# Kernel tuning notes

Measured on AMD Instinct MI355X. Metric: run time of the kernel, lower is better.

Reference implementation:

```python
import jax, jax.numpy as jnp
import numpy as np

B = 16384
TEXT_D = 768
TECH_D = 256
IN_D = TEXT_D + TECH_D  # 1024
OUT_D = 1024
E = 8


def setup_inputs() -> dict:
    key = jax.random.key(0)
    ks = jax.random.split(key, 8)
    s_in = 1.0 / np.sqrt(IN_D)
    s_out = 1.0 / np.sqrt(OUT_D)
    return {
        "text_features": jax.random.normal(ks[0], (B, TEXT_D), jnp.float32),
        "technical_features": jax.random.normal(ks[1], (B, TECH_D), jnp.float32),
        # stacked expert params: layer1 [E, IN_D, OUT_D], layer2 [E, OUT_D, OUT_D]
        "W1": jax.random.uniform(ks[2], (E, IN_D, OUT_D), jnp.float32, -s_in, s_in),
        "b1": jax.random.uniform(ks[3], (E, OUT_D), jnp.float32, -s_in, s_in),
        "W2": jax.random.uniform(ks[4], (E, OUT_D, OUT_D), jnp.float32, -s_out, s_out),
        "b2": jax.random.uniform(ks[5], (E, OUT_D), jnp.float32, -s_out, s_out),
        # gating network
        "Wg": jax.random.uniform(ks[6], (IN_D, E), jnp.float32, -s_in, s_in),
        "bg": jax.random.uniform(ks[7], (E,), jnp.float32, -s_in, s_in),
    }


def reference(text_features, technical_features, W1, b1, W2, b2, Wg, bg):
    x = jnp.concatenate([text_features, technical_features], axis=-1)  # [B, IN_D]
    gates = jax.nn.softmax(x @ Wg + bg, axis=-1)                       # [B, E]
    h = jax.nn.relu(jnp.einsum('bi,eio->beo', x, W1) + b1[None])       # [B, E, OUT_D]
    y = jnp.einsum('beo,eop->bep', h, W2) + b2[None]                   # [B, E, OUT_D]
    return jnp.einsum('be,bep->bp', gates, y)                          # [B, OUT_D]
```

## Files before the change

kernel.cpp:

```cpp
#include <hip/hip_runtime.h>
#include <hip/hip_bf16.h>

#define NB 16384
#define TEXT_D 768
#define TECH_D 256
#define IND 1024
#define OUTD 1024
#define NE 8
#define KH2 4096

typedef unsigned short u16;
typedef __bf16 bf16x8 __attribute__((ext_vector_type(8)));
typedef float f32x4 __attribute__((ext_vector_type(4)));

__device__ __forceinline__ u16 f2bf(float f) {
  union { float f; unsigned int u; } x; x.f = f;
  unsigned int u = x.u;
  return (u16)((u + 0x7FFFu + ((u >> 16) & 1u)) >> 16);
}

__device__ __forceinline__ void gload_lds16(const void* g, void* l) {
  __builtin_amdgcn_global_load_lds(
      (const __attribute__((address_space(1))) unsigned int*)g,
      (__attribute__((address_space(3))) unsigned int*)l, 16, 0, 0);
}

__global__ __launch_bounds__(256) void convert_gates(
    const float* __restrict__ text, const float* __restrict__ tech,
    const float* __restrict__ Wg, const float* __restrict__ bg,
    u16* __restrict__ xb, float* __restrict__ gates) {
  int t = threadIdx.x;
  int wave = t >> 6, lane = t & 63;
  int row = blockIdx.x * 4 + wave;

  float acc[NE];
#pragma unroll
  for (int e = 0; e < NE; ++e) acc[e] = 0.f;

#pragma unroll
  for (int j = 0; j < 4; ++j) {
    int col = j * 256 + lane * 4;
    float4 v = (j < 3) ? *(const float4*)&text[(size_t)row * TEXT_D + col]
                       : *(const float4*)&tech[(size_t)row * TECH_D + lane * 4];
    ushort4 o = make_ushort4(f2bf(v.x), f2bf(v.y), f2bf(v.z), f2bf(v.w));
    *(ushort4*)&xb[(size_t)row * IND + col] = o;
    const float* wp = &Wg[(size_t)col * NE];
    float xv[4] = {v.x, v.y, v.z, v.w};
#pragma unroll
    for (int i = 0; i < 4; ++i) {
      float4 w0 = *(const float4*)&wp[i * NE];
      float4 w1 = *(const float4*)&wp[i * NE + 4];
      acc[0] = fmaf(xv[i], w0.x, acc[0]);
      acc[1] = fmaf(xv[i], w0.y, acc[1]);
      acc[2] = fmaf(xv[i], w0.z, acc[2]);
      acc[3] = fmaf(xv[i], w0.w, acc[3]);
      acc[4] = fmaf(xv[i], w1.x, acc[4]);
      acc[5] = fmaf(xv[i], w1.y, acc[5]);
      acc[6] = fmaf(xv[i], w1.z, acc[6]);
      acc[7] = fmaf(xv[i], w1.w, acc[7]);
    }
  }
#pragma unroll
  for (int off = 32; off; off >>= 1)
#pragma unroll
    for (int e = 0; e < NE; ++e) acc[e] += __shfl_xor(acc[e], off);

#pragma unroll
  for (int e = 0; e < NE; ++e) acc[e] += bg[e];
  float mx = acc[0];
#pragma unroll
  for (int e = 1; e < NE; ++e) mx = fmaxf(mx, acc[e]);
  float s = 0.f;
#pragma unroll
  for (int e = 0; e < NE; ++e) { acc[e] = expf(acc[e] - mx); s += acc[e]; }
  float inv = 1.f / s;
  if (lane < NE) gates[(size_t)row * NE + lane] = acc[lane] * inv;
}

__global__ __launch_bounds__(256) void transpose_w12(
    const float* __restrict__ W1, const float* __restrict__ W2,
    u16* __restrict__ W1t, u16* __restrict__ W2t) {
  __shared__ u16 tile[64][65];
  int bid = blockIdx.x;
  int half = bid >> 11;
  int b2 = bid & 2047;
  int e = b2 >> 8;
  int tb = b2 & 255;
  int r0 = (tb >> 4) * 64;
  int c0 = (tb & 15) * 64;
  const float* We; u16* Wte; int ostride;
  if (half == 0) {
    We = W1 + (size_t)e * IND * OUTD;
    Wte = W1t + ((size_t)e << 20);
    ostride = 1024;
  } else {
    We = W2 + (size_t)e * IND * OUTD;
    Wte = W2t + ((size_t)(e >> 2) << 22) + (size_t)(e & 3) * 1024;
    ostride = KH2;
  }
  int t = threadIdx.x;
  int tr = t >> 4;
  int s  = t & 15;
  int tc = s * 4;
#pragma unroll
  for (int j = 0; j < 4; ++j) {
    int row = j * 16 + tr;
    float4 v = *(const float4*)&We[(size_t)(r0 + row) * OUTD + c0 + tc];
    tile[row][tc + 0] = f2bf(v.x);
    tile[row][tc + 1] = f2bf(v.y);
    tile[row][tc + 2] = f2bf(v.z);
    tile[row][tc + 3] = f2bf(v.w);
  }
  __syncthreads();
#pragma unroll
  for (int j = 0; j < 4; ++j) {
    int row = j * 16 + tr;
    ushort4 o;
    if (half == 0) {
      o = make_ushort4(tile[tc + 0][row], tile[tc + 1][row],
                       tile[tc + 2][row], tile[tc + 3][row]);
    } else {
      o = make_ushort4(tile[s][row], tile[s + 16][row],
                       tile[s + 32][row], tile[s + 48][row]);
    }
    *(ushort4*)&Wte[(size_t)(c0 + row) * ostride + r0 + tc] = o;
  }
}

#define BAR() asm volatile("s_barrier" ::: "memory")
#define VM0() asm volatile("s_waitcnt vmcnt(0)" ::: "memory")
#define VM2() asm volatile("s_waitcnt vmcnt(2)" ::: "memory")
#define VM6() asm volatile("s_waitcnt vmcnt(6)" ::: "memory")

template <int SLOT, int K>
__device__ __forceinline__ void stage_slot(
    const u16* __restrict__ g, char* buf, int k0,
    int ch0, int rsub, int koff, int lbyte) {
#pragma unroll
  for (int j = 0; j < 2; ++j) {
    int ch = ch0 + j;
    int r;
    if constexpr (SLOT == 0)      r = (ch >> 3) * 128 + (ch & 7) * 8 + rsub;
    else if constexpr (SLOT == 3) r = 64 + (ch >> 3) * 128 + (ch & 7) * 8 + rsub;
    else if constexpr (SLOT == 1) r = (ch >> 2) * 64 + (ch & 3) * 8 + rsub;
    else                          r = (ch >> 2) * 64 + 32 + (ch & 3) * 8 + rsub;
    gload_lds16(g + (size_t)r * K + k0 + koff, buf + r * 128 + lbyte);
  }
}

template <int QH>
__device__ __forceinline__ void load_a(const char* rb, int wr, int lr, int hi,
                                       int swr, bf16x8 (&a)[4][2]) {
#pragma unroll
  for (int i = 0; i < 4; ++i)
#pragma unroll
    for (int ks = 0; ks < 2; ++ks)
      a[i][ks] = *(const bf16x8*)(rb + (wr * 128 + QH * 64 + i * 16 + lr) * 128
                                  + ((ks * 64 + hi * 16) ^ swr));
}

template <int NH>
__device__ __forceinline__ void load_b(const char* rb, int wc, int lr, int hi,
                                       int swr, bf16x8 (&b)[2][2]) {
#pragma unroll
  for (int q = 0; q < 2; ++q)
#pragma unroll
    for (int ks = 0; ks < 2; ++ks)
      b[q][ks] = *(const bf16x8*)(rb +
                                  (wc * 64 + (NH * 2 + q) * 16 + lr) * 128
                                  + ((ks * 64 + hi * 16) ^ swr));
}

template <int MH, int NH>
__device__ __forceinline__ void mfma_quad(const bf16x8 (&a)[4][2],
                                          const bf16x8 (&b)[2][2],
                                          f32x4 (&acc)[8][4]) {
#pragma unroll
  for (int i = 0; i < 4; ++i)
#pragma unroll
    for (int q = 0; q < 2; ++q) {
      acc[MH*4+i][NH*2+q] = __builtin_amdgcn_mfma_f32_16x16x32_bf16(
          a[i][0], b[q][0], acc[MH*4+i][NH*2+q], 0, 0, 0);
      acc[MH*4+i][NH*2+q] = __builtin_amdgcn_mfma_f32_16x16x32_bf16(
          a[i][1], b[q][1], acc[MH*4+i][NH*2+q], 0, 0, 0);
    }
}

template <bool LAST, int K>
__device__ __forceinline__ void tile_body(
    const u16* __restrict__ pA, const u16* __restrict__ pB,
    const char* rA, const char* rB, char* sA, char* sB, int kN,
    int ch0, int rsub, int koff, int lbyte,
    int wr, int wc, int lr, int hi, int swr,
    bf16x8 (&a)[4][2], bf16x8 (&b0)[2][2], bf16x8 (&b1)[2][2],
    f32x4 (&acc)[8][4]) {
  if constexpr (!LAST) {
    stage_slot<0, K>(pA, sA, kN, ch0, rsub, koff, lbyte);
    stage_slot<1, K>(pB, sB, kN, ch0, rsub, koff, lbyte);
    stage_slot<2, K>(pB, sB, kN, ch0, rsub, koff, lbyte);
  }
  load_a<0>(rA, wr, lr, hi, swr, a);
  load_b<0>(rB, wc, lr, hi, swr, b0);
  load_b<1>(rB, wc, lr, hi, swr, b1);
  __builtin_amdgcn_s_setprio(1);
  mfma_quad<0, 0>(a, b0, acc);
  mfma_quad<0, 1>(a, b1, acc);
  __builtin_amdgcn_s_setprio(0);
  if constexpr (!LAST) { VM6(); } else { VM0(); }
  BAR();
  if constexpr (!LAST)
    stage_slot<3, K>(pA, sA, kN, ch0, rsub, koff, lbyte);
  load_a<1>(rA, wr, lr, hi, swr, a);
  __builtin_amdgcn_s_setprio(1);
  mfma_quad<1, 0>(a, b0, acc);
  mfma_quad<1, 1>(a, b1, acc);
  __builtin_amdgcn_s_setprio(0);
  if constexpr (!LAST) { VM2(); BAR(); }
}

template <int K>
__device__ __forceinline__ void core256(const u16* __restrict__ pA,
                                        const u16* __restrict__ pB,
                                        char* lds, int t, f32x4 (&acc)[8][4]) {
  constexpr int KT = K / 64;
  static_assert(KT >= 2, "KT must be >= 2");
  const int l = t & 63;
  const int w = t >> 6;
  const int wr = w >> 2, wc = w & 3;
  const int lr = l & 15, hi = l >> 4;
  const int rsub = l >> 3;
  const int koff = ((l & 7) ^ rsub) << 3;
  const int lbyte = (l & 7) * 16;
  const int ch0 = w * 2;
  const int swr = (lr & 7) << 4;

  char* A0 = lds;
  char* A1 = lds + 32768;
  char* B0 = lds + 65536;
  char* B1 = lds + 98304;

  bf16x8 a[4][2], b0[2][2], b1[2][2];

  stage_slot<0, K>(pA, A0, 0, ch0, rsub, koff, lbyte);
  stage_slot<1, K>(pB, B0, 0, ch0, rsub, koff, lbyte);
  stage_slot<2, K>(pB, B0, 0, ch0, rsub, koff, lbyte);
  stage_slot<3, K>(pA, A0, 0, ch0, rsub, koff, lbyte);
  VM0(); BAR();

  char *rA = A0, *rB = B0, *sA = A1, *sB = B1;
  for (int T = 0; T < KT - 1; ++T) {
    tile_body<false, K>(pA, pB, rA, rB, sA, sB, (T + 1) * 64,
                        ch0, rsub, koff, lbyte, wr, wc, lr, hi, swr,
                        a, b0, b1, acc);
    char* x = rA; rA = sA; sA = x;
    x = rB; rB = sB; sB = x;
  }
  tile_body<true, K>(pA, pB, rA, rB, sA, sB, 0,
                     ch0, rsub, koff, lbyte, wr, wc, lr, hi, swr,
                     a, b0, b1, acc);
}

__global__ __launch_bounds__(512, 2) void gemm1(
    const u16* __restrict__ xb, const u16* __restrict__ W1t,
    const float* __restrict__ b1, const float* __restrict__ gates,
    u16* __restrict__ Hg, int eg0) {
  __shared__ char lds[131072];
  int t = threadIdx.x;
  int nwg = gridDim.x, cpx = nwg >> 3, bid = blockIdx.x;
  int swz = (bid & 7) * cpx + (bid >> 3);
  int nb = swz & 3, ee = (swz >> 2) & 3, mb = swz >> 4;
  int e = eg0 + ee;

  f32x4 acc[8][4] = {};
  core256<1024>(xb + (size_t)mb * 256 * 1024,
                W1t + ((size_t)e << 20) + (size_t)nb * 256 * 1024,
                lds, t, acc);

  int l = t & 63, w = t >> 6, wr = w >> 2, wc = w & 3, lr = l & 15, hi = l >> 4;
  int m0 = mb * 256 + wr * 128 + hi * 4;
  int n0 = nb * 256 + wc * 64 + lr;
  int nst = nb * 256 + wc * 64 + lr * 4;
  const float* b1e = b1 + e * OUTD;
  float bv[4];
#pragma unroll
  for (int nn = 0; nn < 4; ++nn) bv[nn] = b1e[n0 + nn * 16];
#pragma unroll
  for (int m = 0; m < 8; ++m) {
#pragma unroll
    for (int r = 0; r < 4; ++r) {
      int row = m0 + m * 16 + r;
      float g = gates[(size_t)row * NE + e];
      ushort4 o;
      o.x = f2bf(g * fmaxf(acc[m][0][r] + bv[0], 0.f));
      o.y = f2bf(g * fmaxf(acc[m][1][r] + bv[1], 0.f));
      o.z = f2bf(g * fmaxf(acc[m][2][r] + bv[2], 0.f));
      o.w = f2bf(g * fmaxf(acc[m][3][r] + bv[3], 0.f));
      *(ushort4*)&Hg[(size_t)row * KH2 + ee * 1024 + nst] = o;
    }
  }
}

template <bool FIRST>
__global__ __launch_bounds__(512, 2) void gemm2(
    const u16* __restrict__ Hg, const u16* __restrict__ W2th,
    const float* __restrict__ b2h, const float* __restrict__ gates,
    float* __restrict__ out, int eg0) {
  __shared__ char lds[131072];
  int t = threadIdx.x;
  int nwg = gridDim.x, cpx = nwg >> 3, bid = blockIdx.x;
  int swz = (bid & 7) * cpx + (bid >> 3);
  int nb = swz & 3, mb = swz >> 2;

  f32x4 acc[8][4] = {};
  core256<KH2>(Hg + (size_t)mb * 256 * KH2, W2th + (size_t)nb * 256 * KH2,
               lds, t, acc);

  int l = t & 63, w = t >> 6, wr = w >> 2, wc = w & 3, lr = l & 15, hi = l >> 4;
  int m0 = mb * 256 + wr * 128 + hi * 4;
  int n0 = nb * 256 + wc * 64 + lr;

  float bcol[4][4];
#pragma unroll
  for (int nn = 0; nn < 4; ++nn)
#pragma unroll
    for (int j = 0; j < 4; ++j)
      bcol[nn][j] = b2h[j * OUTD + n0 + nn * 16];

#pragma unroll
  for (int m = 0; m < 8; ++m) {
#pragma unroll
    for (int r = 0; r < 4; ++r) {
      int row = m0 + m * 16 + r;
      float4 ga = *(const float4*)&gates[(size_t)row * NE + eg0];
#pragma unroll
      for (int nn = 0; nn < 4; ++nn) {
        float bias = ga.x * bcol[nn][0] + ga.y * bcol[nn][1] +
                     ga.z * bcol[nn][2] + ga.w * bcol[nn][3];
        size_t oi = (size_t)row * OUTD + n0 + nn * 16;
        float v = acc[m][nn][r] + bias;
        if (FIRST) out[oi] = v;
        else       out[oi] += v;
      }
    }
  }
}

extern "C" void kernel_launch(void* const* d_in, const int* in_sizes, int n_in,
                              void* d_out, int out_size, void* d_ws, size_t ws_size,
                              hipStream_t stream) {
  (void)in_sizes; (void)n_in; (void)out_size; (void)ws_size;
  const float* text = (const float*)d_in[0];
  const float* tech = (const float*)d_in[1];
  const float* W1   = (const float*)d_in[2];
  const float* b1   = (const float*)d_in[3];
  const float* W2   = (const float*)d_in[4];
  const float* b2   = (const float*)d_in[5];
  const float* Wg   = (const float*)d_in[6];
  const float* bg   = (const float*)d_in[7];
  float* out = (float*)d_out;

  char* p = (char*)d_ws;
  u16* xb  = (u16*)p;  p += (size_t)NB * IND * 2;
  u16* W1t = (u16*)p;  p += (size_t)NE * IND * OUTD * 2;
  u16* W2t = (u16*)p;  p += (size_t)NE * OUTD * OUTD * 2;
  float* gates = (float*)p; p += (size_t)NB * NE * 4;
  u16* Hg  = (u16*)p;

  convert_gates<<<dim3(NB / 4), dim3(256), 0, stream>>>(text, tech, Wg, bg, xb, gates);
  transpose_w12<<<dim3(4096), dim3(256), 0, stream>>>(W1, W2, W1t, W2t);

  for (int h = 0; h < 2; ++h) {
    int eg0 = h * 4;
    gemm1<<<dim3(1024), dim3(512), 0, stream>>>(xb, W1t, b1, gates, Hg, eg0);
    const u16* W2th = W2t + ((size_t)h << 22);
    const float* b2h = b2 + (size_t)eg0 * OUTD;
    if (h == 0)
      gemm2<true><<<dim3(256), dim3(512), 0, stream>>>(Hg, W2th, b2h, gates, out, eg0);
    else
      gemm2<false><<<dim3(256), dim3(512), 0, stream>>>(Hg, W2th, b2h, gates, out, eg0);
  }
}
```

Baseline: 581.1 us.

## Load A operand directly from global into registers, stage only B in LDS

The GEMM core stops staging the A tile through LDS. Each wave now loads its A fragments straight from global memory into registers, double-buffered across the two M-halves, while only B is staged via global_load_lds, which halves LDS use. The aim is to cut LDS traffic and one barrier per tile. The cost is no A reuse across the four column waves: each A row is fetched by four waves, which raises global and L2 traffic and register pressure. The vmcnt accounting also becomes harder to get right.

```diff
diff --git a/kernel.cpp b/kernel.cpp
--- a/kernel.cpp
+++ b/kernel.cpp
@@ -128,9 +128,30 @@
 }
 
 #define BAR() asm volatile("s_barrier" ::: "memory")
-#define VM0() asm volatile("s_waitcnt vmcnt(0)" ::: "memory")
-#define VM2() asm volatile("s_waitcnt vmcnt(2)" ::: "memory")
-#define VM6() asm volatile("s_waitcnt vmcnt(6)" ::: "memory")
+#define VM8() asm volatile("s_waitcnt vmcnt(8)" ::: "memory")
+#define FENCE()                                  \
+  do {                                           \
+    asm volatile("" ::: "memory");               \
+    __builtin_amdgcn_sched_barrier(0);           \
+  } while (0)
+
+struct AP { const u16* p[2][4]; };
+
+__device__ __forceinline__ void advance_ap(AP& ap) {
+#pragma unroll
+  for (int q = 0; q < 2; ++q)
+#pragma unroll
+    for (int i = 0; i < 4; ++i) ap.p[q][i] += 64;
+}
+
+template <int QH>
+__device__ __forceinline__ void load_a_glb(const AP& ap, bf16x8 (&a)[4][2]) {
+#pragma unroll
+  for (int i = 0; i < 4; ++i)
+#pragma unroll
+    for (int ks = 0; ks < 2; ++ks)
+      a[i][ks] = *(const bf16x8*)(ap.p[QH][i] + ks * 32);
+}
 
 template <int SLOT, int K>
 __device__ __forceinline__ void stage_slot(
@@ -140,23 +161,10 @@
   for (int j = 0; j < 2; ++j) {
     int ch = ch0 + j;
     int r;
-    if constexpr (SLOT == 0)      r = (ch >> 3) * 128 + (ch & 7) * 8 + rsub;
-    else if constexpr (SLOT == 3) r = 64 + (ch >> 3) * 128 + (ch & 7) * 8 + rsub;
-    else if constexpr (SLOT == 1) r = (ch >> 2) * 64 + (ch & 3) * 8 + rsub;
-    else                          r = (ch >> 2) * 64 + 32 + (ch & 3) * 8 + rsub;
+    if constexpr (SLOT == 1) r = (ch >> 2) * 64 + (ch & 3) * 8 + rsub;
+    else                     r = (ch >> 2) * 64 + 32 + (ch & 3) * 8 + rsub;
     gload_lds16(g + (size_t)r * K + k0 + koff, buf + r * 128 + lbyte);
   }
-}
-
-template <int QH>
-__device__ __forceinline__ void load_a(const char* rb, int wr, int lr, int hi,
-                                       int swr, bf16x8 (&a)[4][2]) {
-#pragma unroll
-  for (int i = 0; i < 4; ++i)
-#pragma unroll
-    for (int ks = 0; ks < 2; ++ks)
-      a[i][ks] = *(const bf16x8*)(rb + (wr * 128 + QH * 64 + i * 16 + lr) * 128
-                                  + ((ks * 64 + hi * 16) ^ swr));
 }
 
 template <int NH>
@@ -188,34 +196,35 @@
 
 template <bool LAST, int K>
 __device__ __forceinline__ void tile_body(
-    const u16* __restrict__ pA, const u16* __restrict__ pB,
-    const char* rA, const char* rB, char* sA, char* sB, int kN,
-    int ch0, int rsub, int koff, int lbyte,
-    int wr, int wc, int lr, int hi, int swr,
-    bf16x8 (&a)[4][2], bf16x8 (&b0)[2][2], bf16x8 (&b1)[2][2],
+    const u16* __restrict__ pB, const char* rB, char* sB, int kN,
+    AP& ap, int ch0, int rsub, int koff, int lbyte,
+    int wc, int lr, int hi, int swr,
+    bf16x8 (&aH0)[4][2], bf16x8 (&aH1)[4][2],
+    bf16x8 (&b0)[2][2], bf16x8 (&b1)[2][2],
     f32x4 (&acc)[8][4]) {
   if constexpr (!LAST) {
-    stage_slot<0, K>(pA, sA, kN, ch0, rsub, koff, lbyte);
     stage_slot<1, K>(pB, sB, kN, ch0, rsub, koff, lbyte);
     stage_slot<2, K>(pB, sB, kN, ch0, rsub, koff, lbyte);
   }
-  load_a<0>(rA, wr, lr, hi, swr, a);
+  FENCE();
+  load_a_glb<1>(ap, aH1);
   load_b<0>(rB, wc, lr, hi, swr, b0);
   load_b<1>(rB, wc, lr, hi, swr, b1);
   __builtin_amdgcn_s_setprio(1);
-  mfma_quad<0, 0>(a, b0, acc);
-  mfma_quad<0, 1>(a, b1, acc);
+  mfma_quad<0, 0>(aH0, b0, acc);
+  mfma_quad<0, 1>(aH0, b1, acc);
   __builtin_amdgcn_s_setprio(0);
-  if constexpr (!LAST) { VM6(); } else { VM0(); }
+  __builtin_amdgcn_sched_barrier(0);
+  if constexpr (!LAST) {
+    advance_ap(ap);
+    load_a_glb<0>(ap, aH0);
+  }
+  __builtin_amdgcn_sched_barrier(0);
+  __builtin_amdgcn_s_setprio(1);
+  mfma_quad<1, 0>(aH1, b0, acc);
+  mfma_quad<1, 1>(aH1, b1, acc);
+  __builtin_amdgcn_s_setprio(0);
   BAR();
-  if constexpr (!LAST)
-    stage_slot<3, K>(pA, sA, kN, ch0, rsub, koff, lbyte);
-  load_a<1>(rA, wr, lr, hi, swr, a);
-  __builtin_amdgcn_s_setprio(1);
-  mfma_quad<1, 0>(a, b0, acc);
-  mfma_quad<1, 1>(a, b1, acc);
-  __builtin_amdgcn_s_setprio(0);
-  if constexpr (!LAST) { VM2(); BAR(); }
 }
 
 template <int K>
@@ -234,37 +243,39 @@
   const int ch0 = w * 2;
   const int swr = (lr & 7) << 4;
 
-  char* A0 = lds;
-  char* A1 = lds + 32768;
-  char* B0 = lds + 65536;
-  char* B1 = lds + 98304;
-
-  bf16x8 a[4][2], b0[2][2], b1[2][2];
-
-  stage_slot<0, K>(pA, A0, 0, ch0, rsub, koff, lbyte);
+  char* B0 = lds;
+  char* B1 = lds + 32768;
+
+  AP ap;
+#pragma unroll
+  for (int q = 0; q < 2; ++q)
+#pragma unroll
+    for (int i = 0; i < 4; ++i)
+      ap.p[q][i] = pA + (size_t)(wr * 128 + q * 64 + i * 16 + lr) * K + hi * 8;
+
+  bf16x8 aH0[4][2], aH1[4][2], b0[2][2], b1[2][2];
+
   stage_slot<1, K>(pB, B0, 0, ch0, rsub, koff, lbyte);
   stage_slot<2, K>(pB, B0, 0, ch0, rsub, koff, lbyte);
-  stage_slot<3, K>(pA, A0, 0, ch0, rsub, koff, lbyte);
-  VM0(); BAR();
-
-  char *rA = A0, *rB = B0, *sA = A1, *sB = B1;
+  FENCE();
+  load_a_glb<0>(ap, aH0);
+  VM8(); BAR();
+
+  char* rB = B0; char* sB = B1;
   for (int T = 0; T < KT - 1; ++T) {
-    tile_body<false, K>(pA, pB, rA, rB, sA, sB, (T + 1) * 64,
-                        ch0, rsub, koff, lbyte, wr, wc, lr, hi, swr,
-                        a, b0, b1, acc);
-    char* x = rA; rA = sA; sA = x;
-    x = rB; rB = sB; sB = x;
-  }
-  tile_body<true, K>(pA, pB, rA, rB, sA, sB, 0,
-                     ch0, rsub, koff, lbyte, wr, wc, lr, hi, swr,
-                     a, b0, b1, acc);
+    tile_body<false, K>(pB, rB, sB, (T + 1) * 64, ap, ch0, rsub, koff, lbyte,
+                        wc, lr, hi, swr, aH0, aH1, b0, b1, acc);
+    char* x = rB; rB = sB; sB = x;
+  }
+  tile_body<true, K>(pB, rB, sB, 0, ap, ch0, rsub, koff, lbyte,
+                     wc, lr, hi, swr, aH0, aH1, b0, b1, acc);
 }
 
 __global__ __launch_bounds__(512, 2) void gemm1(
     const u16* __restrict__ xb, const u16* __restrict__ W1t,
     const float* __restrict__ b1, const float* __restrict__ gates,
     u16* __restrict__ Hg, int eg0) {
-  __shared__ char lds[131072];
+  __shared__ char lds[65536];
   int t = threadIdx.x;
   int nwg = gridDim.x, cpx = nwg >> 3, bid = blockIdx.x;
   int swz = (bid & 7) * cpx + (bid >> 3);
@@ -305,7 +316,7 @@
     const u16* __restrict__ Hg, const u16* __restrict__ W2th,
     const float* __restrict__ b2h, const float* __restrict__ gates,
     float* __restrict__ out, int eg0) {
-  __shared__ char lds[131072];
+  __shared__ char lds[65536];
   int t = threadIdx.x;
   int nwg = gridDim.x, cpx = nwg >> 3, bid = blockIdx.x;
   int swz = (bid & 7) * cpx + (bid >> 3);
```

New measurement: 1.125 ms. +93.6%, slower.

## Restructure GEMM main loop into four-phase LDS-read/MFMA ping-pong schedule

Applied to the files above, without the earlier changes.

Splits each K-tile into four MFMA quadrants, each interleaved with LDS fragment reads for the next quadrant and global-to-LDS staging. Register buffers are split into a0/a1 so the next tile's A/B fragments can be prefetched during the last quadrant, and explicit lgkmcnt waits with scheduling barriers fix the order. The goal is to hide LDS read latency behind MFMA work. In exchange it adds more barriers per tile and uses more VGPRs, which may pressure occupancy at 512 threads with two blocks per CU.

```diff
diff --git a/kernel.cpp b/kernel.cpp
--- a/kernel.cpp
+++ b/kernel.cpp
@@ -131,6 +131,11 @@
 #define VM0() asm volatile("s_waitcnt vmcnt(0)" ::: "memory")
 #define VM2() asm volatile("s_waitcnt vmcnt(2)" ::: "memory")
 #define VM6() asm volatile("s_waitcnt vmcnt(6)" ::: "memory")
+#define LG0()                                            \
+  do {                                                   \
+    asm volatile("s_waitcnt lgkmcnt(0)" ::: "memory");   \
+    __builtin_amdgcn_sched_barrier(0);                   \
+  } while (0)
 
 template <int SLOT, int K>
 __device__ __forceinline__ void stage_slot(
@@ -175,6 +180,7 @@
 __device__ __forceinline__ void mfma_quad(const bf16x8 (&a)[4][2],
                                           const bf16x8 (&b)[2][2],
                                           f32x4 (&acc)[8][4]) {
+  __builtin_amdgcn_s_setprio(1);
 #pragma unroll
   for (int i = 0; i < 4; ++i)
 #pragma unroll
@@ -184,38 +190,46 @@
       acc[MH*4+i][NH*2+q] = __builtin_amdgcn_mfma_f32_16x16x32_bf16(
           a[i][1], b[q][1], acc[MH*4+i][NH*2+q], 0, 0, 0);
     }
+  __builtin_amdgcn_s_setprio(0);
 }
 
 template <bool LAST, int K>
-__device__ __forceinline__ void tile_body(
+__device__ __forceinline__ void tile4(
     const u16* __restrict__ pA, const u16* __restrict__ pB,
     const char* rA, const char* rB, char* sA, char* sB, int kN,
     int ch0, int rsub, int koff, int lbyte,
     int wr, int wc, int lr, int hi, int swr,
-    bf16x8 (&a)[4][2], bf16x8 (&b0)[2][2], bf16x8 (&b1)[2][2],
+    bf16x8 (&a0)[4][2], bf16x8 (&a1)[4][2],
+    bf16x8 (&b0)[2][2], bf16x8 (&b1)[2][2],
     f32x4 (&acc)[8][4]) {
+  LG0();
+  mfma_quad<0, 0>(a0, b0, acc);
+  load_b<1>(rB, wc, lr, hi, swr, b1);
   if constexpr (!LAST) {
     stage_slot<0, K>(pA, sA, kN, ch0, rsub, koff, lbyte);
     stage_slot<1, K>(pB, sB, kN, ch0, rsub, koff, lbyte);
     stage_slot<2, K>(pB, sB, kN, ch0, rsub, koff, lbyte);
-  }
-  load_a<0>(rA, wr, lr, hi, swr, a);
-  load_b<0>(rB, wc, lr, hi, swr, b0);
-  load_b<1>(rB, wc, lr, hi, swr, b1);
-  __builtin_amdgcn_s_setprio(1);
-  mfma_quad<0, 0>(a, b0, acc);
-  mfma_quad<0, 1>(a, b1, acc);
-  __builtin_amdgcn_s_setprio(0);
-  if constexpr (!LAST) { VM6(); } else { VM0(); }
+    VM6();
+  } else {
+    VM0();
+  }
   BAR();
+  LG0();
+  mfma_quad<0, 1>(a0, b1, acc);
+  load_a<1>(rA, wr, lr, hi, swr, a1);
   if constexpr (!LAST)
     stage_slot<3, K>(pA, sA, kN, ch0, rsub, koff, lbyte);
-  load_a<1>(rA, wr, lr, hi, swr, a);
-  __builtin_amdgcn_s_setprio(1);
-  mfma_quad<1, 0>(a, b0, acc);
-  mfma_quad<1, 1>(a, b1, acc);
-  __builtin_amdgcn_s_setprio(0);
-  if constexpr (!LAST) { VM2(); BAR(); }
+  BAR();
+  LG0();
+  mfma_quad<1, 0>(a1, b0, acc);
+  if constexpr (!LAST) { VM2(); }
+  BAR();
+  mfma_quad<1, 1>(a1, b1, acc);
+  if constexpr (!LAST) {
+    load_a<0>(sA, wr, lr, hi, swr, a0);
+    load_b<0>(sB, wc, lr, hi, swr, b0);
+  }
+  BAR();
 }
 
 template <int K>
@@ -239,25 +253,27 @@
   char* B0 = lds + 65536;
   char* B1 = lds + 98304;
 
-  bf16x8 a[4][2], b0[2][2], b1[2][2];
+  bf16x8 a0[4][2], a1[4][2], b0[2][2], b1[2][2];
 
   stage_slot<0, K>(pA, A0, 0, ch0, rsub, koff, lbyte);
   stage_slot<1, K>(pB, B0, 0, ch0, rsub, koff, lbyte);
   stage_slot<2, K>(pB, B0, 0, ch0, rsub, koff, lbyte);
   stage_slot<3, K>(pA, A0, 0, ch0, rsub, koff, lbyte);
-  VM0(); BAR();
+  VM2(); BAR();
+  load_a<0>(A0, wr, lr, hi, swr, a0);
+  load_b<0>(B0, wc, lr, hi, swr, b0);
 
   char *rA = A0, *rB = B0, *sA = A1, *sB = B1;
   for (int T = 0; T < KT - 1; ++T) {
-    tile_body<false, K>(pA, pB, rA, rB, sA, sB, (T + 1) * 64,
-                        ch0, rsub, koff, lbyte, wr, wc, lr, hi, swr,
-                        a, b0, b1, acc);
+    tile4<false, K>(pA, pB, rA, rB, sA, sB, (T + 1) * 64,
+                    ch0, rsub, koff, lbyte, wr, wc, lr, hi, swr,
+                    a0, a1, b0, b1, acc);
     char* x = rA; rA = sA; sA = x;
     x = rB; rB = sB; sB = x;
   }
-  tile_body<true, K>(pA, pB, rA, rB, sA, sB, 0,
-                     ch0, rsub, koff, lbyte, wr, wc, lr, hi, swr,
-                     a, b0, b1, acc);
+  tile4<true, K>(pA, pB, rA, rB, sA, sB, 0,
+                 ch0, rsub, koff, lbyte, wr, wc, lr, hi, swr,
+                 a0, a1, b0, b1, acc);
 }
 
 __global__ __launch_bounds__(512, 2) void gemm1(
```

New measurement: 572.0 us (median of 2 runs). Within noise of the previous version (-1.6%).

## Restructure GEMM core to 128x256 tiles with triple-buffered K=32 pipeline

Applied to the files above, without the earlier changes.

Replaces the 256x256 double-buffered GEMM core (512 threads, K-step 64, swizzled LDS) with a 128x256 tile core on 256 threads using a three-stage LDS ring of K=32 slices. The LDS layout becomes k-chunk-major instead of XOR-swizzled. Launch grids double and each wave now holds a 4x8 accumulator block. The aim is deeper prefetch, a smaller LDS footprint and more blocks for occupancy. In exchange each tile gets less operand reuse, there are more barriers per K, and the unswizzled LDS reads may hit bank conflicts.

```diff
diff --git a/kernel.cpp b/kernel.cpp
--- a/kernel.cpp
+++ b/kernel.cpp
@@ -128,216 +128,159 @@
 }
 
 #define BAR() asm volatile("s_barrier" ::: "memory")
-#define VM0() asm volatile("s_waitcnt vmcnt(0)" ::: "memory")
-#define VM2() asm volatile("s_waitcnt vmcnt(2)" ::: "memory")
-#define VM6() asm volatile("s_waitcnt vmcnt(6)" ::: "memory")
-
-template <int SLOT, int K>
-__device__ __forceinline__ void stage_slot(
-    const u16* __restrict__ g, char* buf, int k0,
-    int ch0, int rsub, int koff, int lbyte) {
+#define VM0()  asm volatile("s_waitcnt vmcnt(0)" ::: "memory")
+#define VM6()  asm volatile("s_waitcnt vmcnt(6)" ::: "memory")
+#define VM12() asm volatile("s_waitcnt vmcnt(12)" ::: "memory")
+
+template <int K>
+__device__ __forceinline__ void stage_tile(
+    const u16* __restrict__ pA, const u16* __restrict__ pB,
+    char* lds, int T, int t) {
+  int kb = T * 32;
+  char* base = lds + (T % 3) * 24576;
 #pragma unroll
   for (int j = 0; j < 2; ++j) {
-    int ch = ch0 + j;
-    int r;
-    if constexpr (SLOT == 0)      r = (ch >> 3) * 128 + (ch & 7) * 8 + rsub;
-    else if constexpr (SLOT == 3) r = 64 + (ch >> 3) * 128 + (ch & 7) * 8 + rsub;
-    else if constexpr (SLOT == 1) r = (ch >> 2) * 64 + (ch & 3) * 8 + rsub;
-    else                          r = (ch >> 2) * 64 + 32 + (ch & 3) * 8 + rsub;
-    gload_lds16(g + (size_t)r * K + k0 + koff, buf + r * 128 + lbyte);
-  }
-}
-
-template <int QH>
-__device__ __forceinline__ void load_a(const char* rb, int wr, int lr, int hi,
-                                       int swr, bf16x8 (&a)[4][2]) {
-#pragma unroll
-  for (int i = 0; i < 4; ++i)
-#pragma unroll
-    for (int ks = 0; ks < 2; ++ks)
-      a[i][ks] = *(const bf16x8*)(rb + (wr * 128 + QH * 64 + i * 16 + lr) * 128
-                                  + ((ks * 64 + hi * 16) ^ swr));
-}
-
-template <int NH>
-__device__ __forceinline__ void load_b(const char* rb, int wc, int lr, int hi,
-                                       int swr, bf16x8 (&b)[2][2]) {
-#pragma unroll
-  for (int q = 0; q < 2; ++q)
-#pragma unroll
-    for (int ks = 0; ks < 2; ++ks)
-      b[q][ks] = *(const bf16x8*)(rb +
-                                  (wc * 64 + (NH * 2 + q) * 16 + lr) * 128
-                                  + ((ks * 64 + hi * 16) ^ swr));
-}
-
-template <int MH, int NH>
-__device__ __forceinline__ void mfma_quad(const bf16x8 (&a)[4][2],
-                                          const bf16x8 (&b)[2][2],
-                                          f32x4 (&acc)[8][4]) {
-#pragma unroll
-  for (int i = 0; i < 4; ++i)
-#pragma unroll
-    for (int q = 0; q < 2; ++q) {
-      acc[MH*4+i][NH*2+q] = __builtin_amdgcn_mfma_f32_16x16x32_bf16(
-          a[i][0], b[q][0], acc[MH*4+i][NH*2+q], 0, 0, 0);
-      acc[MH*4+i][NH*2+q] = __builtin_amdgcn_mfma_f32_16x16x32_bf16(
-          a[i][1], b[q][1], acc[MH*4+i][NH*2+q], 0, 0, 0);
-    }
-}
-
-template <bool LAST, int K>
-__device__ __forceinline__ void tile_body(
-    const u16* __restrict__ pA, const u16* __restrict__ pB,
-    const char* rA, const char* rB, char* sA, char* sB, int kN,
-    int ch0, int rsub, int koff, int lbyte,
-    int wr, int wc, int lr, int hi, int swr,
-    bf16x8 (&a)[4][2], bf16x8 (&b0)[2][2], bf16x8 (&b1)[2][2],
-    f32x4 (&acc)[8][4]) {
-  if constexpr (!LAST) {
-    stage_slot<0, K>(pA, sA, kN, ch0, rsub, koff, lbyte);
-    stage_slot<1, K>(pB, sB, kN, ch0, rsub, koff, lbyte);
-    stage_slot<2, K>(pB, sB, kN, ch0, rsub, koff, lbyte);
-  }
-  load_a<0>(rA, wr, lr, hi, swr, a);
-  load_b<0>(rB, wc, lr, hi, swr, b0);
-  load_b<1>(rB, wc, lr, hi, swr, b1);
-  __builtin_amdgcn_s_setprio(1);
-  mfma_quad<0, 0>(a, b0, acc);
-  mfma_quad<0, 1>(a, b1, acc);
-  __builtin_amdgcn_s_setprio(0);
-  if constexpr (!LAST) { VM6(); } else { VM0(); }
-  BAR();
-  if constexpr (!LAST)
-    stage_slot<3, K>(pA, sA, kN, ch0, rsub, koff, lbyte);
-  load_a<1>(rA, wr, lr, hi, swr, a);
-  __builtin_amdgcn_s_setprio(1);
-  mfma_quad<1, 0>(a, b0, acc);
-  mfma_quad<1, 1>(a, b1, acc);
-  __builtin_amdgcn_s_setprio(0);
-  if constexpr (!LAST) { VM2(); BAR(); }
+    int d = t + 256 * j;
+    gload_lds16(pA + (size_t)(d & 127) * K + kb + (d >> 7) * 8, base + d * 16);
+  }
+#pragma unroll
+  for (int j = 0; j < 4; ++j)
+    gload_lds16(pB + (size_t)t * K + kb + j * 8,
+                base + 8192 + (t + 256 * j) * 16);
 }
 
 template <int K>
-__device__ __forceinline__ void core256(const u16* __restrict__ pA,
-                                        const u16* __restrict__ pB,
-                                        char* lds, int t, f32x4 (&acc)[8][4]) {
-  constexpr int KT = K / 64;
-  static_assert(KT >= 2, "KT must be >= 2");
+__device__ __forceinline__ void core128x256(const u16* __restrict__ pA,
+                                            const u16* __restrict__ pB,
+                                            char* lds, int t,
+                                            f32x4 (&acc)[4][8]) {
+  constexpr int KT = K / 32;
+  static_assert(KT >= 2, "KT >= 2");
   const int l = t & 63;
   const int w = t >> 6;
-  const int wr = w >> 2, wc = w & 3;
+  const int wr = w >> 1, wc = w & 1;
   const int lr = l & 15, hi = l >> 4;
-  const int rsub = l >> 3;
-  const int koff = ((l & 7) ^ rsub) << 3;
-  const int lbyte = (l & 7) * 16;
-  const int ch0 = w * 2;
-  const int swr = (lr & 7) << 4;
-
-  char* A0 = lds;
-  char* A1 = lds + 32768;
-  char* B0 = lds + 65536;
-  char* B1 = lds + 98304;
-
-  bf16x8 a[4][2], b0[2][2], b1[2][2];
-
-  stage_slot<0, K>(pA, A0, 0, ch0, rsub, koff, lbyte);
-  stage_slot<1, K>(pB, B0, 0, ch0, rsub, koff, lbyte);
-  stage_slot<2, K>(pB, B0, 0, ch0, rsub, koff, lbyte);
-  stage_slot<3, K>(pA, A0, 0, ch0, rsub, koff, lbyte);
-  VM0(); BAR();
-
-  char *rA = A0, *rB = B0, *sA = A1, *sB = B1;
-  for (int T = 0; T < KT - 1; ++T) {
-    tile_body<false, K>(pA, pB, rA, rB, sA, sB, (T + 1) * 64,
-                        ch0, rsub, koff, lbyte, wr, wc, lr, hi, swr,
-                        a, b0, b1, acc);
-    char* x = rA; rA = sA; sA = x;
-    x = rB; rB = sB; sB = x;
-  }
-  tile_body<true, K>(pA, pB, rA, rB, sA, sB, 0,
-                     ch0, rsub, koff, lbyte, wr, wc, lr, hi, swr,
-                     a, b0, b1, acc);
-}
-
-__global__ __launch_bounds__(512, 2) void gemm1(
+
+  stage_tile<K>(pA, pB, lds, 0, t);
+  stage_tile<K>(pA, pB, lds, 1, t);
+
+  for (int T = 0; T < KT; ++T) {
+    if (T + 2 < KT) {
+      stage_tile<K>(pA, pB, lds, T + 2, t);
+      VM12();
+    } else if (T + 1 < KT) {
+      VM6();
+    } else {
+      VM0();
+    }
+    BAR();
+    const char* rb = lds + (T % 3) * 24576;
+    bf16x8 a[4], b[8];
+#pragma unroll
+    for (int i = 0; i < 4; ++i)
+      a[i] = *(const bf16x8*)(rb + hi * 2048 + (wr * 64 + i * 16 + lr) * 16);
+#pragma unroll
+    for (int n = 0; n < 8; ++n)
+      b[n] = *(const bf16x8*)(rb + 8192 + hi * 4096 +
+                              (wc * 128 + n * 16 + lr) * 16);
+    __builtin_amdgcn_s_setprio(1);
+#pragma unroll
+    for (int i = 0; i < 4; ++i)
+#pragma unroll
+      for (int n = 0; n < 8; ++n)
+        acc[i][n] = __builtin_amdgcn_mfma_f32_16x16x32_bf16(a[i], b[n],
+                                                            acc[i][n], 0, 0, 0);
+    __builtin_amdgcn_s_setprio(0);
+    BAR();
+  }
+}
+
+__global__ __launch_bounds__(256, 2) void gemm1(
     const u16* __restrict__ xb, const u16* __restrict__ W1t,
     const float* __restrict__ b1, const float* __restrict__ gates,
     u16* __restrict__ Hg, int eg0) {
-  __shared__ char lds[131072];
+  __shared__ char lds[73728];
   int t = threadIdx.x;
   int nwg = gridDim.x, cpx = nwg >> 3, bid = blockIdx.x;
   int swz = (bid & 7) * cpx + (bid >> 3);
-  int nb = swz & 3, ee = (swz >> 2) & 3, mb = swz >> 4;
+  int nt = swz & 15, mb = swz >> 4;
+
+  int colbase = nt * 256;
+  int ee = colbase >> 10;
   int e = eg0 + ee;
 
-  f32x4 acc[8][4] = {};
-  core256<1024>(xb + (size_t)mb * 256 * 1024,
-                W1t + ((size_t)e << 20) + (size_t)nb * 256 * 1024,
-                lds, t, acc);
-
-  int l = t & 63, w = t >> 6, wr = w >> 2, wc = w & 3, lr = l & 15, hi = l >> 4;
-  int m0 = mb * 256 + wr * 128 + hi * 4;
-  int n0 = nb * 256 + wc * 64 + lr;
-  int nst = nb * 256 + wc * 64 + lr * 4;
+  f32x4 acc[4][8] = {};
+  core128x256<1024>(xb + (size_t)mb * 128 * 1024,
+                    W1t + ((size_t)e << 20) + (size_t)(colbase & 1023) * 1024,
+                    lds, t, acc);
+
+  int l = t & 63, w = t >> 6, wr = w >> 1, wc = w & 1, lr = l & 15, hi = l >> 4;
+  int m0 = mb * 128 + wr * 64 + hi * 4;
+  int ne0 = (colbase & 1023) + wc * 128;
   const float* b1e = b1 + e * OUTD;
-  float bv[4];
-#pragma unroll
-  for (int nn = 0; nn < 4; ++nn) bv[nn] = b1e[n0 + nn * 16];
-#pragma unroll
-  for (int m = 0; m < 8; ++m) {
+  float bv[8];
+#pragma unroll
+  for (int nn = 0; nn < 8; ++nn) bv[nn] = b1e[ne0 + nn * 16 + lr];
+#pragma unroll
+  for (int i = 0; i < 4; ++i) {
 #pragma unroll
     for (int r = 0; r < 4; ++r) {
-      int row = m0 + m * 16 + r;
+      int row = m0 + i * 16 + r;
       float g = gates[(size_t)row * NE + e];
-      ushort4 o;
-      o.x = f2bf(g * fmaxf(acc[m][0][r] + bv[0], 0.f));
-      o.y = f2bf(g * fmaxf(acc[m][1][r] + bv[1], 0.f));
-      o.z = f2bf(g * fmaxf(acc[m][2][r] + bv[2], 0.f));
-      o.w = f2bf(g * fmaxf(acc[m][3][r] + bv[3], 0.f));
-      *(ushort4*)&Hg[(size_t)row * KH2 + ee * 1024 + nst] = o;
+      ushort4 o1, o2;
+      o1.x = f2bf(g * fmaxf(acc[i][0][r] + bv[0], 0.f));
+      o1.y = f2bf(g * fmaxf(acc[i][1][r] + bv[1], 0.f));
+      o1.z = f2bf(g * fmaxf(acc[i][2][r] + bv[2], 0.f));
+      o1.w = f2bf(g * fmaxf(acc[i][3][r] + bv[3], 0.f));
+      o2.x = f2bf(g * fmaxf(acc[i][4][r] + bv[4], 0.f));
+      o2.y = f2bf(g * fmaxf(acc[i][5][r] + bv[5], 0.f));
+      o2.z = f2bf(g * fmaxf(acc[i][6][r] + bv[6], 0.f));
+      o2.w = f2bf(g * fmaxf(acc[i][7][r] + bv[7], 0.f));
+      size_t base = (size_t)row * KH2 + ee * 1024 + ne0;
+      *(ushort4*)&Hg[base + 4 * lr]      = o1;
+      *(ushort4*)&Hg[base + 64 + 4 * lr] = o2;
     }
   }
 }
 
 template <bool FIRST>
-__global__ __launch_bounds__(512, 2) void gemm2(
+__global__ __launch_bounds__(256, 2) void gemm2(
     const u16* __restrict__ Hg, const u16* __restrict__ W2th,
     const float* __restrict__ b2h, const float* __restrict__ gates,
     float* __restrict__ out, int eg0) {
-  __shared__ char lds[131072];
+  __shared__ char lds[73728];
   int t = threadIdx.x;
   int nwg = gridDim.x, cpx = nwg >> 3, bid = blockIdx.x;
   int swz = (bid & 7) * cpx + (bid >> 3);
-  int nb = swz & 3, mb = swz >> 2;
-
-  f32x4 acc[8][4] = {};
-  core256<KH2>(Hg + (size_t)mb * 256 * KH2, W2th + (size_t)nb * 256 * KH2,
-               lds, t, acc);
-
-  int l = t & 63, w = t >> 6, wr = w >> 2, wc = w & 3, lr = l & 15, hi = l >> 4;
-  int m0 = mb * 256 + wr * 128 + hi * 4;
-  int n0 = nb * 256 + wc * 64 + lr;
-
-  float bcol[4][4];
-#pragma unroll
-  for (int nn = 0; nn < 4; ++nn)
+  int nt = swz & 3, mb = swz >> 2;
+
+  f32x4 acc[4][8] = {};
+  core128x256<KH2>(Hg + (size_t)mb * 128 * KH2,
+                   W2th + (size_t)nt * 256 * KH2, lds, t, acc);
+
+  int l = t & 63, w = t >> 6, wr = w >> 1, wc = w & 1, lr = l & 15, hi = l >> 4;
+  int m0 = mb * 128 + wr * 64 + hi * 4;
+  int n0 = nt * 256 + wc * 128 + lr;
+
+  float bcol[8][4];
+#pragma unroll
+  for (int nn = 0; nn < 8; ++nn)
 #pragma unroll
     for (int j = 0; j < 4; ++j)
       bcol[nn][j] = b2h[j * OUTD + n0 + nn * 16];
 
 #pragma unroll
-  for (int m = 0; m < 8; ++m) {
+  for (int i = 0; i < 4; ++i) {
 #pragma unroll
     for (int r = 0; r < 4; ++r) {
-      int row = m0 + m * 16 + r;
+      int row = m0 + i * 16 + r;
       float4 ga = *(const float4*)&gates[(size_t)row * NE + eg0];
 #pragma unroll
-      for (int nn = 0; nn < 4; ++nn) {
+      for (int nn = 0; nn < 8; ++nn) {
         float bias = ga.x * bcol[nn][0] + ga.y * bcol[nn][1] +
                      ga.z * bcol[nn][2] + ga.w * bcol[nn][3];
         size_t oi = (size_t)row * OUTD + n0 + nn * 16;
-        float v = acc[m][nn][r] + bias;
+        float v = acc[i][nn][r] + bias;
         if (FIRST) out[oi] = v;
         else       out[oi] += v;
       }
@@ -371,12 +314,12 @@
 
   for (int h = 0; h < 2; ++h) {
     int eg0 = h * 4;
-    gemm1<<<dim3(1024), dim3(512), 0, stream>>>(xb, W1t, b1, gates, Hg, eg0);
+    gemm1<<<dim3(2048), dim3(256), 0, stream>>>(xb, W1t, b1, gates, Hg, eg0);
     const u16* W2th = W2t + ((size_t)h << 22);
     const float* b2h = b2 + (size_t)eg0 * OUTD;
     if (h == 0)
-      gemm2<true><<<dim3(256), dim3(512), 0, stream>>>(Hg, W2th, b2h, gates, out, eg0);
+      gemm2<true><<<dim3(512), dim3(256), 0, stream>>>(Hg, W2th, b2h, gates, out, eg0);
     else
-      gemm2<false><<<dim3(256), dim3(512), 0, stream>>>(Hg, W2th, b2h, gates, out, eg0);
-  }
-}
+      gemm2<false><<<dim3(512), dim3(256), 0, stream>>>(Hg, W2th, b2h, gates, out, eg0);
+  }
+}
```

Measured after the change: 978.0 us. 1.68x slower.
